# Performance work log

Measured on AMD Instinct MI355X. Metric: run time of the kernel, lower is better.

The kernel has to match this reference:

```python
import jax, jax.numpy as jnp
import numpy as np

K = 3   # spatial_kernel_size
M = 5   # memory_size


def setup_inputs() -> dict:
    key = jax.random.key(0)
    ks = jax.random.split(key, 16)
    C = 64
    B, H, D, W = 2, 24, 24, 24
    s = 0.05
    n = jax.random.normal
    return {
        "x": n(ks[0], (B, C, H, D, W), jnp.float32),
        "prev_memory": jnp.zeros((B, C), jnp.float32),
        "Wq": n(ks[1], (C, C), jnp.float32) * s,
        "bq": n(ks[2], (C,), jnp.float32) * s,
        "Wk": n(ks[3], (C, C), jnp.float32) * s,
        "bk": n(ks[4], (C,), jnp.float32) * s,
        "Wv": n(ks[5], (C, C), jnp.float32) * s,
        "bv": n(ks[6], (C,), jnp.float32) * s,
        "mem_key": n(ks[7], (C, M), jnp.float32),
        "mem_value": n(ks[8], (C, M), jnp.float32),
        "Wg": n(ks[9], (C, 2 * C), jnp.float32) * s,
        "bg": n(ks[10], (C,), jnp.float32) * s,
        "W_ih": n(ks[11], (3 * C, C), jnp.float32) * s,
        "W_hh": n(ks[12], (3 * C, C), jnp.float32) * s,
        "b_ih": n(ks[13], (3 * C,), jnp.float32) * s,
        "b_hh": n(ks[14], (3 * C,), jnp.float32) * s,
    }


def _patches(x, k):
    # x: (B,C,H,D,W) -> (B,C,k^3,H,D,W) local neighborhoods (zero-padded)
    B, C, H, D, W = x.shape
    p = k // 2
    xp = jnp.pad(x, ((0, 0), (0, 0), (p, p), (p, p), (p, p)))
    sl = [xp[:, :, i:i + H, j:j + D, l:l + W]
          for i in range(k) for j in range(k) for l in range(k)]
    return jnp.stack(sl, axis=2)


def reference(x, prev_memory, Wq, bq, Wk, bk, Wv, bv, mem_key, mem_value,
              Wg, bg, W_ih, W_hh, b_ih, b_hh):
    B, C, H, D, W = x.shape
    N = H * D * W
    xf = x.reshape(B, C, N)
    pf = _patches(x, K).reshape(B, C, K ** 3, N)

    # 1x1x1 conv projections (pure channel mixes)
    q = jnp.einsum('oc,bcn->bon', Wq, xf) + bq[None, :, None]            # (B,C,N)
    k_sp = jnp.einsum('oc,bcmn->bomn', Wk, pf) + bk[None, :, None, None]  # (B,C,27,N)
    v_sp = jnp.einsum('oc,bcmn->bomn', Wv, pf) + bv[None, :, None, None]

    # memory tokens broadcast over all spatial locations
    k_mem = jnp.broadcast_to(mem_key[None, :, :, None], (B, C, M, N))
    v_mem = jnp.broadcast_to(mem_value[None, :, :, None], (B, C, M, N))
    kk = jnp.concatenate([k_mem, k_sp], axis=2)   # (B,C,M+27,N)
    vv = jnp.concatenate([v_mem, v_sp], axis=2)

    # per-channel scalar attention over memory+neighborhood axis
    attn = jax.nn.softmax(q[:, :, None, :] * kk / jnp.sqrt(jnp.float32(C)), axis=2)
    out = jnp.sum(attn * vv, axis=2).reshape(B, C, H, D, W)

    # sigmoid gate over concat([x, out])
    gin = jnp.concatenate([xf, out.reshape(B, C, N)], axis=1)  # (B,2C,N)
    gate = jax.nn.sigmoid(jnp.einsum('oc,bcn->bon', Wg, gin)
                          + bg[None, :, None]).reshape(B, C, H, D, W)
    out = gate * out + (1.0 - gate) * x

    # GRU memory update on spatially pooled features (torch GRUCell math)
    mu = out.mean(axis=(2, 3, 4))                 # (B,C)
    gi = mu @ W_ih.T + b_ih
    gh = prev_memory @ W_hh.T + b_hh
    ir, iz, ii = jnp.split(gi, 3, axis=1)
    hr, hz, hn = jnp.split(gh, 3, axis=1)
    r = jax.nn.sigmoid(ir + hr)
    z = jax.nn.sigmoid(iz + hz)
    ng = jnp.tanh(ii + r * hn)
    new_memory = (1.0 - z) * ng + z * prev_memory
    return out, new_memory
```

## Files before the change

kernel.cpp:

```cpp
#include <hip/hip_runtime.h>
#include <math.h>

#define NPOS 13824
#define CDIM 64
#define BTCH 2
#define LOG2E 1.4426950408889634f
#define QSCALE (0.125f * LOG2E)

__device__ __forceinline__ unsigned int f2bf1(float f) {
  unsigned int u = __float_as_uint(f);
  return (u + 0x7FFFu + ((u >> 16) & 1u)) >> 16;
}

__global__ __launch_bounds__(256) void qkvg_kernel(
    const float* __restrict__ x,
    const float* __restrict__ Wq, const float* __restrict__ bq,
    const float* __restrict__ Wk, const float* __restrict__ bk,
    const float* __restrict__ Wv, const float* __restrict__ bv,
    const float* __restrict__ Wg,
    float* __restrict__ Qb, unsigned int* __restrict__ KVp,
    float* __restrict__ GXT, float* __restrict__ pool)
{
  __shared__ __align__(16) float wqt[64*68];
  __shared__ __align__(16) float wkt[64*68];
  __shared__ __align__(16) float wvt[64*68];
  __shared__ __align__(16) float wgt[64*68];
  const int t  = threadIdx.x;
  const int bi = blockIdx.x;
  const int b  = bi / 216;
  const int n0 = (bi - b*216) * 64;
  if (bi == 0 && t < 128) pool[t] = 0.0f;

  #pragma unroll
  for (int k = 0; k < 16; ++k) {
    int idx = t + k*256;
    int lo = idx & 63, hi = idx >> 6;
    wqt[lo*68 + hi] = Wq[idx] * QSCALE;
    wkt[lo*68 + hi] = Wk[idx];
    wvt[lo*68 + hi] = Wv[idx];
    wgt[lo*68 + hi] = Wg[hi*128 + lo];
  }
  __syncthreads();

  const int c0  = (t & 15) * 4;
  const int nn0 = (t >> 4) * 4;
  const float* xbase = x + (size_t)(b*64)*NPOS + n0 + nn0;
  float aq[4][4] = {}; float ak[4][4] = {}; float av[4][4] = {}; float ag[4][4] = {};
  #pragma unroll 4
  for (int cp = 0; cp < 64; ++cp) {
    const float4 xv4 = *(const float4*)(xbase + (size_t)cp*NPOS);
    const float4 q4  = *(const float4*)&wqt[cp*68 + c0];
    const float4 k4  = *(const float4*)&wkt[cp*68 + c0];
    const float4 v4  = *(const float4*)&wvt[cp*68 + c0];
    const float4 g4  = *(const float4*)&wgt[cp*68 + c0];
    const float xa[4] = {xv4.x, xv4.y, xv4.z, xv4.w};
    const float qa[4] = {q4.x, q4.y, q4.z, q4.w};
    const float ka[4] = {k4.x, k4.y, k4.z, k4.w};
    const float va[4] = {v4.x, v4.y, v4.z, v4.w};
    const float ga[4] = {g4.x, g4.y, g4.z, g4.w};
    #pragma unroll
    for (int ci = 0; ci < 4; ++ci)
      #pragma unroll
      for (int ni = 0; ni < 4; ++ni) {
        aq[ci][ni] = fmaf(qa[ci], xa[ni], aq[ci][ni]);
        ak[ci][ni] = fmaf(ka[ci], xa[ni], ak[ci][ni]);
        av[ci][ni] = fmaf(va[ci], xa[ni], av[ci][ni]);
        ag[ci][ni] = fmaf(ga[ci], xa[ni], ag[ci][ni]);
      }
  }
  float4 xr[4];
  #pragma unroll
  for (int e = 0; e < 4; ++e)
    xr[e] = *(const float4*)(x + (size_t)(b*64 + c0 + e)*NPOS + n0 + nn0);
  const float xre[4][4] = {{xr[0].x,xr[0].y,xr[0].z,xr[0].w},
                           {xr[1].x,xr[1].y,xr[1].z,xr[1].w},
                           {xr[2].x,xr[2].y,xr[2].z,xr[2].w},
                           {xr[3].x,xr[3].y,xr[3].z,xr[3].w}};
  const float4 bq4 = *(const float4*)&bq[c0];
  const float4 bk4 = *(const float4*)&bk[c0];
  const float4 bv4 = *(const float4*)&bv[c0];
  #pragma unroll
  for (int ni = 0; ni < 4; ++ni) {
    const int p = b*NPOS + n0 + nn0 + ni;
    float4 o;
    o = make_float4(fmaf(bq4.x,QSCALE,aq[0][ni]), fmaf(bq4.y,QSCALE,aq[1][ni]),
                    fmaf(bq4.z,QSCALE,aq[2][ni]), fmaf(bq4.w,QSCALE,aq[3][ni]));
    *(float4*)&Qb[p*64 + c0] = o;
    uint4 kv;
    kv.x = (f2bf1(ak[0][ni]+bk4.x) << 16) | f2bf1(av[0][ni]+bv4.x);
    kv.y = (f2bf1(ak[1][ni]+bk4.y) << 16) | f2bf1(av[1][ni]+bv4.y);
    kv.z = (f2bf1(ak[2][ni]+bk4.z) << 16) | f2bf1(av[2][ni]+bv4.z);
    kv.w = (f2bf1(ak[3][ni]+bk4.w) << 16) | f2bf1(av[3][ni]+bv4.w);
    *(uint4*)&KVp[p*64 + c0] = kv;
    o = make_float4(ag[0][ni], xre[0][ni], ag[1][ni], xre[1][ni]);
    *(float4*)&GXT[(size_t)(p*64 + c0)*2]     = o;
    o = make_float4(ag[2][ni], xre[2][ni], ag[3][ni], xre[3][ni]);
    *(float4*)&GXT[(size_t)(p*64 + c0)*2 + 4] = o;
  }
}

__global__ __launch_bounds__(256, 4) void attn_kernel(
    float* __restrict__ QOT,
    const unsigned int* __restrict__ KVp,
    const float* __restrict__ GXT,
    const float* __restrict__ bk, const float* __restrict__ bv,
    const float* __restrict__ memk, const float* __restrict__ memv,
    const float* __restrict__ Wg, const float* __restrict__ bg,
    float* __restrict__ pool)
{
  __shared__ __align__(16) unsigned int kvbuf[8000];
  __shared__ __align__(16) float alsA[256];
  __shared__ __align__(16) float alsB[256];
  const int t = threadIdx.x;
  const int c = t & 63;
  const int w = t >> 6;

  {
    float* wgt2 = (float*)kvbuf;
    #pragma unroll
    for (int k = 0; k < 16; ++k) {
      int u = t + k*256;
      int cp = u >> 6, j = u & 63;
      wgt2[j*65 + cp] = Wg[cp*128 + 64 + j];
    }
  }
  __syncthreads();
  unsigned int wg2p[32];
  {
    const float* wgt2 = (const float*)kvbuf;
    #pragma unroll
    for (int j2 = 0; j2 < 32; ++j2) {
      unsigned lo = f2bf1(wgt2[(2*j2)*65 + c]);
      unsigned hi = f2bf1(wgt2[(2*j2+1)*65 + c]);
      wg2p[j2] = lo | (hi << 16);
    }
  }
  float mk[5], mv[5];
  #pragma unroll
  for (int m = 0; m < 5; ++m) { mk[m] = memk[c*5 + m]; mv[m] = memv[c*5 + m]; }
  const float bg_c = bg[c];
  __syncthreads();

  const int bi = (int)(blockIdx.x & 7) * 128 + (int)(blockIdx.x >> 3);
  const int b  = bi >> 9;
  const int tb = bi & 511;
  const int h0 = (tb >> 6) * 3;
  const int d0 = ((tb >> 3) & 7) * 3;
  const int w0 = (tb & 7) * 3;
  const int bN = b * NPOS;

  for (int u = t; u < 125*16; u += 256) {
    int pos = u >> 4, q4 = u & 15;
    int ph = pos / 25, pr = pos - ph*25;
    int pd = pr / 5,  pw = pr - pd*5;
    int hh = h0 - 1 + ph, dd = d0 - 1 + pd, ww = w0 - 1 + pw;
    bool inb = ((unsigned)hh < 24u) && ((unsigned)dd < 24u) && ((unsigned)ww < 24u);
    uint4 kv;
    if (inb) {
      kv = *(const uint4*)(KVp + ((size_t)(bN + hh*576 + dd*24 + ww))*64 + q4*4);
    } else {
      const float4 kf = ((const float4*)bk)[q4];
      const float4 vf = ((const float4*)bv)[q4];
      kv.x = (f2bf1(kf.x) << 16) | f2bf1(vf.x);
      kv.y = (f2bf1(kf.y) << 16) | f2bf1(vf.y);
      kv.z = (f2bf1(kf.z) << 16) | f2bf1(vf.z);
      kv.w = (f2bf1(kf.w) << 16) | f2bf1(vf.w);
    }
    *(uint4*)&kvbuf[pos*64 + q4*4] = kv;
  }
  __syncthreads();

  float pacc = 0.0f;
  for (int li = w; li < 27; li += 8) {
    const int liB0 = li + 4;
    const bool hasB = liB0 < 27;
    const int liB = hasB ? liB0 : li;

    const int lhA = li / 9,  lrA = li - lhA*9;
    const int ldA = lrA / 3, lwA = lrA - ldA*3;
    const int pA  = bN + (h0+lhA)*576 + (d0+ldA)*24 + (w0+lwA);
    const int hbA = (lhA*25 + ldA*5 + lwA)*64 + c;
    const int lhB = liB / 9,  lrB = liB - lhB*9;
    const int ldB = lrB / 3,  lwB = lrB - ldB*3;
    const int pB  = bN + (h0+lhB)*576 + (d0+ldB)*24 + (w0+lwB);
    const int hbB = (lhB*25 + ldB*5 + lwB)*64 + c;

    const float qA = QOT[pA*64 + c];
    const float qB = QOT[pB*64 + c];
    const float2 gxA = *(const float2*)&GXT[(size_t)(pA*64 + c)*2];
    const float2 gxB = *(const float2*)&GXT[(size_t)(pB*64 + c)*2];

    float sA0 = 0.f, sA1 = 0.f, oA0 = 0.f, oA1 = 0.f;
    float sB0 = 0.f, sB1 = 0.f, oB0 = 0.f, oB1 = 0.f;
    #pragma unroll
    for (int m = 0; m < 5; ++m) {
      const float pfA = __builtin_amdgcn_exp2f(qA * mk[m]);
      const float pfB = __builtin_amdgcn_exp2f(qB * mk[m]);
      if (m & 1) { sA1 += pfA; oA1 = fmaf(pfA, mv[m], oA1);
                   sB1 += pfB; oB1 = fmaf(pfB, mv[m], oB1); }
      else       { sA0 += pfA; oA0 = fmaf(pfA, mv[m], oA0);
                   sB0 += pfB; oB0 = fmaf(pfB, mv[m], oB0); }
    }
    const unsigned int* kvA = &kvbuf[hbA];
    const unsigned int* kvB = &kvbuf[hbB];
    #pragma unroll
    for (int i = 0; i < 3; ++i)
      #pragma unroll
      for (int j = 0; j < 3; ++j)
        #pragma unroll
        for (int l = 0; l < 3; ++l) {
          const int s4  = i*9 + j*3 + l;
          const int off = (i*25 + j*5 + l)*64;
          const unsigned a = kvA[off], bb2 = kvB[off];
          const float kA = __uint_as_float(a & 0xFFFF0000u);
          const float vA = __uint_as_float(a << 16);
          const float kB = __uint_as_float(bb2 & 0xFFFF0000u);
          const float vB = __uint_as_float(bb2 << 16);
          const float pfA = __builtin_amdgcn_exp2f(qA * kA);
          const float pfB = __builtin_amdgcn_exp2f(qB * kB);
          if (s4 & 1) { sA1 += pfA; oA1 = fmaf(pfA, vA, oA1);
                        sB1 += pfB; oB1 = fmaf(pfB, vB, oB1); }
          else        { sA0 += pfA; oA0 = fmaf(pfA, vA, oA0);
                        sB0 += pfB; oB0 = fmaf(pfB, vB, oB0); }
        }
    const float attA = (oA0 + oA1) * __builtin_amdgcn_rcpf(sA0 + sA1);
    const float attB = (oB0 + oB1) * __builtin_amdgcn_rcpf(sB0 + sB1);

    alsA[w*64 + c] = attA;
    alsB[w*64 + c] = attB;
    float gA0 = gxA.x + bg_c, gA1 = 0.f, gA2 = 0.f, gA3 = 0.f;
    float gB0 = gxB.x + bg_c, gB1 = 0.f, gB2 = 0.f, gB3 = 0.f;
    #pragma unroll
    for (int j4 = 0; j4 < 16; ++j4) {
      const float4 a4 = *(const float4*)&alsA[w*64 + j4*4];
      const float4 b4 = *(const float4*)&alsB[w*64 + j4*4];
      const unsigned pk0 = wg2p[2*j4], pk1 = wg2p[2*j4+1];
      const float w0f = __uint_as_float(pk0 << 16);
      const float w1f = __uint_as_float(pk0 & 0xFFFF0000u);
      const float w2f = __uint_as_float(pk1 << 16);
      const float w3f = __uint_as_float(pk1 & 0xFFFF0000u);
      gA0 = fmaf(w0f, a4.x, gA0); gB0 = fmaf(w0f, b4.x, gB0);
      gA1 = fmaf(w1f, a4.y, gA1); gB1 = fmaf(w1f, b4.y, gB1);
      gA2 = fmaf(w2f, a4.z, gA2); gB2 = fmaf(w2f, b4.z, gB2);
      gA3 = fmaf(w3f, a4.w, gA3); gB3 = fmaf(w3f, b4.w, gB3);
    }
    const float glA   = (gA0 + gA1) + (gA2 + gA3);
    const float glB   = (gB0 + gB1) + (gB2 + gB3);
    const float gateA = __builtin_amdgcn_rcpf(1.0f + __builtin_amdgcn_exp2f(-LOG2E * glA));
    const float gateB = __builtin_amdgcn_rcpf(1.0f + __builtin_amdgcn_exp2f(-LOG2E * glB));
    const float finA  = fmaf(gateA, attA - gxA.y, gxA.y);
    const float finB  = fmaf(gateB, attB - gxB.y, gxB.y);
    QOT[pA*64 + c] = finA;
    pacc += finA;
    if (hasB) { QOT[pB*64 + c] = finB; pacc += finB; }
  }

  alsA[t] = pacc;
  __syncthreads();
  if (t < 64) {
    float s = alsA[t] + alsA[64 + t] + alsA[128 + t] + alsA[192 + t];
    atomicAdd(&pool[b*64 + t], s);
  }
}

__global__ __launch_bounds__(256) void outpool_kernel(
    const float* __restrict__ OT, float* __restrict__ out,
    const float* __restrict__ pool, const float* __restrict__ prev,
    const float* __restrict__ W_ih, const float* __restrict__ W_hh,
    const float* __restrict__ b_ih, const float* __restrict__ b_hh,
    float* __restrict__ outmem)
{
  __shared__ __align__(16) float ls[64*65];
  __shared__ __align__(16) float mu[128];
  __shared__ float gi[384];
  __shared__ float gh[384];
  const int t  = threadIdx.x;
  const int bi = blockIdx.x;
  const int b  = bi / 216;
  const int n0 = (bi - b*216) * 64;
  #pragma unroll
  for (int i = 0; i < 16; ++i) {
    int u = i*256 + t;
    int pos = u >> 6, cc = u & 63;
    ls[cc*65 + pos] = OT[(size_t)(b*NPOS + n0 + pos)*64 + cc];
  }
  if (bi == 0 && t < 128) mu[t] = pool[t] * (1.0f / (float)NPOS);
  __syncthreads();
  #pragma unroll
  for (int i = 0; i < 16; ++i) {
    int u = i*256 + t;
    int cc = u >> 6, j = u & 63;
    out[(size_t)(b*64 + cc)*NPOS + n0 + j] = ls[cc*65 + j];
  }
  if (bi != 0) return;

  for (int r = t; r < 384; r += 256) {
    const int b2 = r / 192, j = r - b2*192;
    const float4* wi4 = (const float4*)(W_ih + (size_t)j*64);
    const float4* wh4 = (const float4*)(W_hh + (size_t)j*64);
    const float4* mu4 = (const float4*)(mu + b2*64);
    const float4* pv4 = (const float4*)(prev + b2*64);
    float sgi = b_ih[j], sgh = b_hh[j];
    #pragma unroll
    for (int k = 0; k < 16; ++k) {
      float4 wv = wi4[k], m4 = mu4[k];
      sgi = fmaf(wv.x, m4.x, sgi); sgi = fmaf(wv.y, m4.y, sgi);
      sgi = fmaf(wv.z, m4.z, sgi); sgi = fmaf(wv.w, m4.w, sgi);
      float4 hv = wh4[k], p4 = pv4[k];
      sgh = fmaf(hv.x, p4.x, sgh); sgh = fmaf(hv.y, p4.y, sgh);
      sgh = fmaf(hv.z, p4.z, sgh); sgh = fmaf(hv.w, p4.w, sgh);
    }
    gi[r] = sgi; gh[r] = sgh;
  }
  __syncthreads();
  if (t < 128) {
    const int b2 = t >> 6, cc = t & 63;
    float ir = gi[b2*192 + cc],       hr = gh[b2*192 + cc];
    float iz = gi[b2*192 + 64 + cc],  hz = gh[b2*192 + 64 + cc];
    float ii = gi[b2*192 + 128 + cc], hn = gh[b2*192 + 128 + cc];
    float rr = 1.0f / (1.0f + __builtin_amdgcn_exp2f(-LOG2E * (ir + hr)));
    float zz = 1.0f / (1.0f + __builtin_amdgcn_exp2f(-LOG2E * (iz + hz)));
    float ng = tanhf(ii + rr * hn);
    outmem[t] = (1.0f - zz) * ng + zz * prev[t];
  }
}

extern "C" void kernel_launch(void* const* d_in, const int* in_sizes, int n_in,
                              void* d_out, int out_size, void* d_ws, size_t ws_size,
                              hipStream_t stream) {
  const float* x    = (const float*)d_in[0];
  const float* prev = (const float*)d_in[1];
  const float* Wq   = (const float*)d_in[2];
  const float* bq   = (const float*)d_in[3];
  const float* Wk   = (const float*)d_in[4];
  const float* bk   = (const float*)d_in[5];
  const float* Wv   = (const float*)d_in[6];
  const float* bv   = (const float*)d_in[7];
  const float* memk = (const float*)d_in[8];
  const float* memv = (const float*)d_in[9];
  const float* Wg   = (const float*)d_in[10];
  const float* bg   = (const float*)d_in[11];
  const float* W_ih = (const float*)d_in[12];
  const float* W_hh = (const float*)d_in[13];
  const float* b_ih = (const float*)d_in[14];
  const float* b_hh = (const float*)d_in[15];

  float* out    = (float*)d_out;
  float* outmem = out + (size_t)BTCH*CDIM*NPOS;

  const size_t SZ = (size_t)BTCH*NPOS*CDIM;
  float* wsf       = (float*)d_ws;
  float* Qb        = wsf;
  unsigned int* KVp = (unsigned int*)(wsf + SZ);
  float* GXT       = wsf + 2*SZ;
  float* pool      = wsf + 4*SZ;

  qkvg_kernel<<<BTCH*216, 256, 0, stream>>>(x, Wq, bq, Wk, bk, Wv, bv, Wg,
                                            Qb, KVp, GXT, pool);
  attn_kernel<<<BTCH*512, 256, 0, stream>>>(Qb, KVp, GXT,
                                            bk, bv, memk, memv, Wg, bg, pool);
  outpool_kernel<<<BTCH*216, 256, 0, stream>>>(Qb, out, pool, prev,
                                               W_ih, W_hh, b_ih, b_hh, outmem);
}
```

Before: 153.2 us.

## Compute QKVG projection with fp16 MFMA from swizzled shared-memory tiles

Replaces the scalar FMA channel-mix in qkvg_kernel with 16x16x32 fp16 MFMA instructions. Weights and the x tile are converted to half precision and stored in XOR-swizzled shared memory, and each wave computes one output group (Q, G, or interleaved K/V) and writes it. The goal is to cut the ALU cost of the projection GEMM, but fp16 inputs lose precision compared with the fp32 FMA path. This kernel is only one part of the total time, next to the attention kernel.

```diff
diff --git a/kernel.cpp b/kernel.cpp
--- a/kernel.cpp
+++ b/kernel.cpp
@@ -1,4 +1,5 @@
 #include <hip/hip_runtime.h>
+#include <hip/hip_fp16.h>
 #include <math.h>
 
 #define NPOS 13824
@@ -7,9 +8,18 @@
 #define LOG2E 1.4426950408889634f
 #define QSCALE (0.125f * LOG2E)
 
+typedef _Float16 f16;
+typedef f16 f16x8 __attribute__((ext_vector_type(8)));
+typedef float f32x4 __attribute__((ext_vector_type(4)));
+
 __device__ __forceinline__ unsigned int f2bf1(float f) {
   unsigned int u = __float_as_uint(f);
   return (u + 0x7FFFu + ((u >> 16) & 1u)) >> 16;
+}
+
+__device__ __forceinline__ unsigned int pkh2(float a, float b) {
+  __half2 h = __floats2half2_rn(a, b);
+  return *reinterpret_cast<unsigned int*>(&h);
 }
 
 __global__ __launch_bounds__(256) void qkvg_kernel(
@@ -21,10 +31,8 @@
     float* __restrict__ Qb, unsigned int* __restrict__ KVp,
     float* __restrict__ GXT, float* __restrict__ pool)
 {
-  __shared__ __align__(16) float wqt[64*68];
-  __shared__ __align__(16) float wkt[64*68];
-  __shared__ __align__(16) float wvt[64*68];
-  __shared__ __align__(16) float wgt[64*68];
+  __shared__ __align__(16) unsigned short ws[256*64];
+  __shared__ __align__(16) unsigned short xs[64*64];
   const int t  = threadIdx.x;
   const int bi = blockIdx.x;
   const int b  = bi / 216;
@@ -32,70 +40,132 @@
   if (bi == 0 && t < 128) pool[t] = 0.0f;
 
   #pragma unroll
-  for (int k = 0; k < 16; ++k) {
-    int idx = t + k*256;
-    int lo = idx & 63, hi = idx >> 6;
-    wqt[lo*68 + hi] = Wq[idx] * QSCALE;
-    wkt[lo*68 + hi] = Wk[idx];
-    wvt[lo*68 + hi] = Wv[idx];
-    wgt[lo*68 + hi] = Wg[hi*128 + lo];
-  }
-  __syncthreads();
-
-  const int c0  = (t & 15) * 4;
-  const int nn0 = (t >> 4) * 4;
-  const float* xbase = x + (size_t)(b*64)*NPOS + n0 + nn0;
-  float aq[4][4] = {}; float ak[4][4] = {}; float av[4][4] = {}; float ag[4][4] = {};
-  #pragma unroll 4
-  for (int cp = 0; cp < 64; ++cp) {
-    const float4 xv4 = *(const float4*)(xbase + (size_t)cp*NPOS);
-    const float4 q4  = *(const float4*)&wqt[cp*68 + c0];
-    const float4 k4  = *(const float4*)&wkt[cp*68 + c0];
-    const float4 v4  = *(const float4*)&wvt[cp*68 + c0];
-    const float4 g4  = *(const float4*)&wgt[cp*68 + c0];
-    const float xa[4] = {xv4.x, xv4.y, xv4.z, xv4.w};
-    const float qa[4] = {q4.x, q4.y, q4.z, q4.w};
-    const float ka[4] = {k4.x, k4.y, k4.z, k4.w};
-    const float va[4] = {v4.x, v4.y, v4.z, v4.w};
-    const float ga[4] = {g4.x, g4.y, g4.z, g4.w};
-    #pragma unroll
-    for (int ci = 0; ci < 4; ++ci)
+  for (int k = 0; k < 4; ++k) {
+    const int u  = t + k*256;
+    const int r  = u >> 4;
+    const int i0 = (u & 15) * 4;
+    const float4 q4 = *(const float4*)&Wq[r*64  + i0];
+    const float4 g4 = *(const float4*)&Wg[r*128 + i0];
+    const float4 k4 = *(const float4*)&Wk[r*64  + i0];
+    const float4 v4 = *(const float4*)&Wv[r*64  + i0];
+    {
+      const int rr = r;
+      const int idx = (rr*64 + i0) ^ ((rr & 7) << 3);
+      *(uint2*)&ws[idx] = make_uint2(pkh2(q4.x*QSCALE, q4.y*QSCALE),
+                                     pkh2(q4.z*QSCALE, q4.w*QSCALE));
+    }
+    {
+      const int rr = 64 + r;
+      const int idx = (rr*64 + i0) ^ ((rr & 7) << 3);
+      *(uint2*)&ws[idx] = make_uint2(pkh2(g4.x, g4.y), pkh2(g4.z, g4.w));
+    }
+    {
+      const int rr = 128 + 2*r;
+      const int idx = (rr*64 + i0) ^ ((rr & 7) << 3);
+      *(uint2*)&ws[idx] = make_uint2(pkh2(k4.x, k4.y), pkh2(k4.z, k4.w));
+    }
+    {
+      const int rr = 129 + 2*r;
+      const int idx = (rr*64 + i0) ^ ((rr & 7) << 3);
+      *(uint2*)&ws[idx] = make_uint2(pkh2(v4.x, v4.y), pkh2(v4.z, v4.w));
+    }
+  }
+  {
+    const int p = t & 63;
+    const size_t xb = (size_t)(b*64)*NPOS + n0 + p;
+    #pragma unroll
+    for (int k = 0; k < 8; ++k) {
+      const int ch0 = (t >> 6) * 2 + k * 8;
+      const float a0 = x[xb + (size_t)ch0*NPOS];
+      const float a1 = x[xb + (size_t)(ch0+1)*NPOS];
+      const int idx = (p*64 + ch0) ^ ((p & 7) << 3);
+      *(unsigned int*)&xs[idx] = pkh2(a0, a1);
+    }
+  }
+  __syncthreads();
+
+  const int l   = t & 63;
+  const int w   = t >> 6;
+  const int lr  = l & 15;
+  const int lkb = (l >> 4) * 8;
+  const int swz = (lr & 7) << 3;
+
+  f16x8 Bf[4][2];
+  #pragma unroll
+  for (int nf = 0; nf < 4; ++nf)
+    #pragma unroll
+    for (int kk = 0; kk < 2; ++kk) {
+      const int prow = nf*16 + lr;
+      Bf[nf][kk] = *(const f16x8*)&xs[(prow*64 + kk*32 + lkb) ^ swz];
+    }
+  f16x8 Af[4][2];
+  #pragma unroll
+  for (int f = 0; f < 4; ++f)
+    #pragma unroll
+    for (int kk = 0; kk < 2; ++kk) {
+      const int row = (w*4 + f)*16 + lr;
+      Af[f][kk] = *(const f16x8*)&ws[(row*64 + kk*32 + lkb) ^ swz];
+    }
+  f32x4 acc[4][4];
+  #pragma unroll
+  for (int f = 0; f < 4; ++f)
+    #pragma unroll
+    for (int nf = 0; nf < 4; ++nf) {
+      f32x4 z = {0.f, 0.f, 0.f, 0.f};
+      z = __builtin_amdgcn_mfma_f32_16x16x32_f16(Af[f][0], Bf[nf][0], z, 0, 0, 0);
+      acc[f][nf] = __builtin_amdgcn_mfma_f32_16x16x32_f16(Af[f][1], Bf[nf][1], z, 0, 0, 0);
+    }
+
+  const int rsub  = (l >> 4) * 4;
+  const int pbase = b*NPOS + n0;
+  if (w == 0) {
+    #pragma unroll
+    for (int f = 0; f < 4; ++f) {
+      const int ch0 = f*16 + rsub;
+      const float4 bq4 = *(const float4*)&bq[ch0];
       #pragma unroll
-      for (int ni = 0; ni < 4; ++ni) {
-        aq[ci][ni] = fmaf(qa[ci], xa[ni], aq[ci][ni]);
-        ak[ci][ni] = fmaf(ka[ci], xa[ni], ak[ci][ni]);
-        av[ci][ni] = fmaf(va[ci], xa[ni], av[ci][ni]);
-        ag[ci][ni] = fmaf(ga[ci], xa[ni], ag[ci][ni]);
+      for (int nf = 0; nf < 4; ++nf) {
+        const int p = pbase + nf*16 + lr;
+        const float4 o = make_float4(fmaf(bq4.x, QSCALE, acc[f][nf].x),
+                                     fmaf(bq4.y, QSCALE, acc[f][nf].y),
+                                     fmaf(bq4.z, QSCALE, acc[f][nf].z),
+                                     fmaf(bq4.w, QSCALE, acc[f][nf].w));
+        *(float4*)&Qb[(size_t)p*64 + ch0] = o;
       }
-  }
-  float4 xr[4];
-  #pragma unroll
-  for (int e = 0; e < 4; ++e)
-    xr[e] = *(const float4*)(x + (size_t)(b*64 + c0 + e)*NPOS + n0 + nn0);
-  const float xre[4][4] = {{xr[0].x,xr[0].y,xr[0].z,xr[0].w},
-                           {xr[1].x,xr[1].y,xr[1].z,xr[1].w},
-                           {xr[2].x,xr[2].y,xr[2].z,xr[2].w},
-                           {xr[3].x,xr[3].y,xr[3].z,xr[3].w}};
-  const float4 bq4 = *(const float4*)&bq[c0];
-  const float4 bk4 = *(const float4*)&bk[c0];
-  const float4 bv4 = *(const float4*)&bv[c0];
-  #pragma unroll
-  for (int ni = 0; ni < 4; ++ni) {
-    const int p = b*NPOS + n0 + nn0 + ni;
-    float4 o;
-    o = make_float4(fmaf(bq4.x,QSCALE,aq[0][ni]), fmaf(bq4.y,QSCALE,aq[1][ni]),
-                    fmaf(bq4.z,QSCALE,aq[2][ni]), fmaf(bq4.w,QSCALE,aq[3][ni]));
-    *(float4*)&Qb[p*64 + c0] = o;
-    uint4 kv;
-    kv.x = (f2bf1(ak[0][ni]+bk4.x) << 16) | f2bf1(av[0][ni]+bv4.x);
-    kv.y = (f2bf1(ak[1][ni]+bk4.y) << 16) | f2bf1(av[1][ni]+bv4.y);
-    kv.z = (f2bf1(ak[2][ni]+bk4.z) << 16) | f2bf1(av[2][ni]+bv4.z);
-    kv.w = (f2bf1(ak[3][ni]+bk4.w) << 16) | f2bf1(av[3][ni]+bv4.w);
-    *(uint4*)&KVp[p*64 + c0] = kv;
-    o = make_float4(ag[0][ni], xre[0][ni], ag[1][ni], xre[1][ni]);
-    *(float4*)&GXT[(size_t)(p*64 + c0)*2]     = o;
-    o = make_float4(ag[2][ni], xre[2][ni], ag[3][ni], xre[3][ni]);
-    *(float4*)&GXT[(size_t)(p*64 + c0)*2 + 4] = o;
+    }
+  } else if (w == 1) {
+    #pragma unroll
+    for (int f = 0; f < 4; ++f) {
+      const int ch0 = f*16 + rsub;
+      #pragma unroll
+      for (int nf = 0; nf < 4; ++nf) {
+        const int pl = n0 + nf*16 + lr;
+        const int p  = pbase + nf*16 + lr;
+        const float xv0 = x[(size_t)(b*64 + ch0+0)*NPOS + pl];
+        const float xv1 = x[(size_t)(b*64 + ch0+1)*NPOS + pl];
+        const float xv2 = x[(size_t)(b*64 + ch0+2)*NPOS + pl];
+        const float xv3 = x[(size_t)(b*64 + ch0+3)*NPOS + pl];
+        const float4 o0 = make_float4(acc[f][nf].x, xv0, acc[f][nf].y, xv1);
+        const float4 o1 = make_float4(acc[f][nf].z, xv2, acc[f][nf].w, xv3);
+        *(float4*)&GXT[((size_t)p*64 + ch0)*2]     = o0;
+        *(float4*)&GXT[((size_t)p*64 + ch0)*2 + 4] = o1;
+      }
+    }
+  } else {
+    #pragma unroll
+    for (int f = 0; f < 4; ++f) {
+      const int c0 = (w - 2)*32 + f*8 + (l >> 4)*2;
+      const float2 bk2 = *(const float2*)&bk[c0];
+      const float2 bv2 = *(const float2*)&bv[c0];
+      #pragma unroll
+      for (int nf = 0; nf < 4; ++nf) {
+        const int p = pbase + nf*16 + lr;
+        uint2 kv;
+        kv.x = (f2bf1(acc[f][nf].x + bk2.x) << 16) | f2bf1(acc[f][nf].y + bv2.x);
+        kv.y = (f2bf1(acc[f][nf].z + bk2.y) << 16) | f2bf1(acc[f][nf].w + bv2.y);
+        *(uint2*)&KVp[(size_t)p*64 + c0] = kv;
+      }
+    }
   }
 }
 
```

Result: faster. 141.4 us (-7.7%).
